# Optimization experiments

Measured on AMD Instinct MI355X. Metric: run time of the kernel, lower is better.

The kernel has to match this reference:

```python
import jax, jax.numpy as jnp
import numpy as np

TOKENS = 8192
IN_F = 4096
OUT_F = 4096
ZERO_POINT = 0  # int8 activation zero point (module default)


def setup_inputs() -> dict:
    key = jax.random.key(0)
    k1, k2, k3, k4 = jax.random.split(key, 4)
    # int8-valued activations/weights stored as int32 (same math as torch upcast path)
    x = jax.random.randint(k1, (TOKENS, IN_F), 0, 127, dtype=jnp.int32)
    weight = jax.random.randint(k2, (IN_F, OUT_F), -127, 127, dtype=jnp.int32)
    bias = jax.random.randint(k3, (1, OUT_F), -64, 64, dtype=jnp.int32)
    gemm_scales = jax.random.uniform(k4, (1, OUT_F), dtype=jnp.float32) * 1e-3
    return {"x": x, "weight": weight, "bias": bias, "gemm_scales": gemm_scales}


def reference(x, weight, bias, gemm_scales):
    # adjust_a = (x - zero_point), upcast to float32 like the torch module
    adjust_a = (x - ZERO_POINT).astype(jnp.float32)          # [T, in]
    w = weight.astype(jnp.float32)                           # [in, out]
    gemm_o = (adjust_a @ w + bias.astype(jnp.float32)) * gemm_scales  # [T, out]
    return gemm_o
```

## Files before the change

kernel.cpp:

```cpp
#include <hip/hip_runtime.h>

using i32x4 = __attribute__((ext_vector_type(4))) int;

#define AS3(p) ((__attribute__((address_space(3))) void*)(p))
#define AS1(p) ((const __attribute__((address_space(1))) void*)(p))

constexpr int M = 8192;
constexpr int N = 4096;
constexpr int K = 4096;
constexpr int BK = 64;
constexpr int NT = K / BK;
constexpr int NBUF = 4;

__global__ void pack_a_kernel(const int4* __restrict__ x, unsigned* __restrict__ a8, int nUnits) {
    int stride = gridDim.x * blockDim.x;
    for (int u = blockIdx.x * blockDim.x + threadIdx.x; u < nUnits; u += stride) {
        int4 v = x[u];
        a8[u] = (v.x & 255) | ((v.y & 255) << 8) | ((v.z & 255) << 16) | (v.w << 24);
    }
}

__global__ void pack_wT_kernel(const int* __restrict__ w, char* __restrict__ b8t) {
    __shared__ __align__(16) char T[64][80];
    const int n0 = blockIdx.x * 64;
    const int k0 = blockIdx.y * 64;
    const int tid = threadIdx.x;

    #pragma unroll
    for (int i = 0; i < 4; i++) {
        int u = tid + i * 256;
        int r = u >> 4;
        int c = u & 15;
        int4 v = *(const int4*)&w[(size_t)(k0 + r) * N + n0 + 4 * c];
        T[4 * c + 0][r] = (char)v.x;
        T[4 * c + 1][r] = (char)v.y;
        T[4 * c + 2][r] = (char)v.z;
        T[4 * c + 3][r] = (char)v.w;
    }
    __syncthreads();

    const int n = tid >> 2;
    const int q = tid & 3;
    int4 val = *(const int4*)&T[n][16 * q];
    *(int4*)&b8t[(size_t)(n0 + n) * K + k0 + 16 * q] = val;
}

__global__ __launch_bounds__(512, 1) void gemm_i8_kernel(
    const char* __restrict__ a8, const char* __restrict__ b8t,
    const int* __restrict__ bias, const float* __restrict__ scales,
    float* __restrict__ out)
{
    __shared__ __align__(16) char As[NBUF][256 * BK];
    __shared__ __align__(16) char Bs[NBUF][256 * BK];

    const int tid  = threadIdx.x;
    const int lane = tid & 63;
    const int wid  = tid >> 6;
    const int wr   = wid >> 2;
    const int wc   = wid & 3;

    const int bid = blockIdx.x;
    const int xcd = bid & 7;
    const int l   = bid >> 3;
    const int tm  = (xcd >> 1) * 8 + (l >> 3);
    const int tn  = (xcd & 1) * 8 + (l & 7);
    const size_t brow = (size_t)tm * 256;
    const size_t bcol = (size_t)tn * 256;

    const int srow = tid >> 2;
    const int schS = ((tid & 3) ^ ((tid >> 3) & 3)) << 4;
    const char* aG = a8  + (brow + srow) * (size_t)K + schS;
    const char* bG = b8t + (bcol + srow) * (size_t)K + schS;
    const int ldsW = wid * 1024;

    i32x4 acc[8][4];
    #pragma unroll
    for (int m = 0; m < 8; m++)
        #pragma unroll
        for (int n = 0; n < 4; n++)
            #pragma unroll
            for (int r = 0; r < 4; r++)
                acc[m][n][r] = 0;

    auto stage = [&](int slot, int kt) {
        const char* a = aG + (size_t)kt * BK;
        const char* b = bG + (size_t)kt * BK;
        char* Ad = &As[slot][0] + ldsW;
        char* Bd = &Bs[slot][0] + ldsW;
        __builtin_amdgcn_global_load_lds(AS1(a),                  AS3(Ad),        16, 0, 0);
        __builtin_amdgcn_global_load_lds(AS1(a + (size_t)128*K),  AS3(Ad + 8192), 16, 0, 0);
        __builtin_amdgcn_global_load_lds(AS1(b),                  AS3(Bd),        16, 0, 0);
        __builtin_amdgcn_global_load_lds(AS1(b + (size_t)128*K),  AS3(Bd + 8192), 16, 0, 0);
    };

    const int frow  = lane & 15;
    const int c0sw  = ((lane >> 4) ^ ((frow >> 1) & 3)) << 4;
    const int raOff = wr * 8192 + frow * 64 + c0sw;
    const int rbOff = wc * 4096 + frow * 64 + c0sw;

    stage(0, 0);
    stage(1, 1);
    stage(2, 2);
    asm volatile("s_waitcnt vmcnt(8)" ::: "memory");
    __builtin_amdgcn_s_barrier();

    #pragma unroll 4
    for (int t = 0; t < NT; ++t) {
        const int slot = t & 3;
        if (t + 3 < NT) stage((t + 3) & 3, t + 3);

        const char* Ab = &As[slot][0] + raOff;
        const char* Bb = &Bs[slot][0] + rbOff;

        i32x4 bfr[4], afr[8];
        #pragma unroll
        for (int n = 0; n < 4; ++n)
            bfr[n] = *(const i32x4*)(Bb + n * 1024);
        #pragma unroll
        for (int m = 0; m < 8; ++m)
            afr[m] = *(const i32x4*)(Ab + m * 1024);

        __builtin_amdgcn_s_barrier();

        asm volatile("s_waitcnt lgkmcnt(4)" ::: "memory");
        __builtin_amdgcn_sched_barrier(0);
        __builtin_amdgcn_s_setprio(1);
        #pragma unroll
        for (int m = 0; m < 4; ++m)
            #pragma unroll
            for (int n = 0; n < 4; ++n)
                acc[m][n] = __builtin_amdgcn_mfma_i32_16x16x64_i8(afr[m], bfr[n], acc[m][n], 0, 0, 0);
        __builtin_amdgcn_s_setprio(0);
        __builtin_amdgcn_sched_barrier(0);

        asm volatile("s_waitcnt lgkmcnt(0)" ::: "memory");
        __builtin_amdgcn_sched_barrier(0);
        __builtin_amdgcn_s_setprio(1);
        #pragma unroll
        for (int m = 4; m < 8; ++m)
            #pragma unroll
            for (int n = 0; n < 4; ++n)
                acc[m][n] = __builtin_amdgcn_mfma_i32_16x16x64_i8(afr[m], bfr[n], acc[m][n], 0, 0, 0);
        __builtin_amdgcn_s_setprio(0);
        __builtin_amdgcn_sched_barrier(0);

        if (t <= NT - 4) asm volatile("s_waitcnt vmcnt(8)" ::: "memory");
        else             asm volatile("s_waitcnt vmcnt(0)" ::: "memory");
        __builtin_amdgcn_s_barrier();
    }

    #pragma unroll
    for (int n = 0; n < 4; ++n) {
        const int col = (int)bcol + wc * 64 + n * 16 + (lane & 15);
        const int bv  = bias[col];
        const float sv = scales[col];
        #pragma unroll
        for (int m = 0; m < 8; ++m) {
            const size_t row0 = brow + wr * 128 + m * 16 + ((lane >> 4) << 2);
            float* o = out + row0 * (size_t)N + col;
            #pragma unroll
            for (int r = 0; r < 4; ++r)
                o[(size_t)r * N] = (float)(acc[m][n][r] + bv) * sv;
        }
    }
}

extern "C" void kernel_launch(void* const* d_in, const int* in_sizes, int n_in,
                              void* d_out, int out_size, void* d_ws, size_t ws_size,
                              hipStream_t stream) {
    const int*   x      = (const int*)d_in[0];
    const int*   w      = (const int*)d_in[1];
    const int*   bias   = (const int*)d_in[2];
    const float* scales = (const float*)d_in[3];
    float* out = (float*)d_out;

    char* a8  = (char*)d_ws;
    char* b8t = a8 + (size_t)M * K;

    pack_a_kernel<<<2048, 256, 0, stream>>>((const int4*)x, (unsigned*)a8, M * K / 4);

    dim3 gt(N / 64, K / 64);
    pack_wT_kernel<<<gt, 256, 0, stream>>>(w, b8t);

    gemm_i8_kernel<<<(M / 256) * (N / 256), 512, 0, stream>>>(a8, b8t, bias, scales, out);
}
```

Before: 206.4 us.

## Restructure int8 GEMM mainloop to BK=128 double buffer with interleaved quadrant MFMA phases

Doubles the K tile to 128 and replaces the 4-deep LDS ring with a double buffer. Each iteration is split into four MFMA quadrant phases, with barriers between them and fragment loads interleaved so that A/B reads reuse registers. The next tile's global-to-LDS loads are issued in two halves between phases. The aim is fewer loop iterations, a smaller fragment register footprint, and higher occupancy (launch bounds now allow 2 waves per SIMD). The cost is many more barriers per iteration, a full vmcnt(0) drain at the end of each iteration, and a shallower prefetch distance.

```diff
diff --git a/kernel.cpp b/kernel.cpp
--- a/kernel.cpp
+++ b/kernel.cpp
@@ -8,9 +8,8 @@
 constexpr int M = 8192;
 constexpr int N = 4096;
 constexpr int K = 4096;
-constexpr int BK = 64;
+constexpr int BK = 128;
 constexpr int NT = K / BK;
-constexpr int NBUF = 4;
 
 __global__ void pack_a_kernel(const int4* __restrict__ x, unsigned* __restrict__ a8, int nUnits) {
     int stride = gridDim.x * blockDim.x;
@@ -45,13 +44,13 @@
     *(int4*)&b8t[(size_t)(n0 + n) * K + k0 + 16 * q] = val;
 }
 
-__global__ __launch_bounds__(512, 1) void gemm_i8_kernel(
+__global__ __launch_bounds__(512, 2) void gemm_i8_kernel(
     const char* __restrict__ a8, const char* __restrict__ b8t,
     const int* __restrict__ bias, const float* __restrict__ scales,
     float* __restrict__ out)
 {
-    __shared__ __align__(16) char As[NBUF][256 * BK];
-    __shared__ __align__(16) char Bs[NBUF][256 * BK];
+    __shared__ __align__(16) char As[2][256 * BK];
+    __shared__ __align__(16) char Bs[2][256 * BK];
 
     const int tid  = threadIdx.x;
     const int lane = tid & 63;
@@ -67,11 +66,11 @@
     const size_t brow = (size_t)tm * 256;
     const size_t bcol = (size_t)tn * 256;
 
-    const int srow = tid >> 2;
-    const int schS = ((tid & 3) ^ ((tid >> 3) & 3)) << 4;
-    const char* aG = a8  + (brow + srow) * (size_t)K + schS;
-    const char* bG = b8t + (bcol + srow) * (size_t)K + schS;
-    const int ldsW = wid * 1024;
+    const int srowS = (wid << 3) + (lane >> 3);
+    const int schS  = ((lane & 7) ^ (lane >> 3)) << 4;
+    const char* aGs = a8  + (brow + srowS) * (size_t)K + schS;
+    const char* bGs = b8t + (bcol + srowS) * (size_t)K + schS;
+    const int ldsU = wid * 1024;
 
     i32x4 acc[8][4];
     #pragma unroll
@@ -82,70 +81,108 @@
             for (int r = 0; r < 4; r++)
                 acc[m][n][r] = 0;
 
-    auto stage = [&](int slot, int kt) {
-        const char* a = aG + (size_t)kt * BK;
-        const char* b = bG + (size_t)kt * BK;
-        char* Ad = &As[slot][0] + ldsW;
-        char* Bd = &Bs[slot][0] + ldsW;
-        __builtin_amdgcn_global_load_lds(AS1(a),                  AS3(Ad),        16, 0, 0);
-        __builtin_amdgcn_global_load_lds(AS1(a + (size_t)128*K),  AS3(Ad + 8192), 16, 0, 0);
-        __builtin_amdgcn_global_load_lds(AS1(b),                  AS3(Bd),        16, 0, 0);
-        __builtin_amdgcn_global_load_lds(AS1(b + (size_t)128*K),  AS3(Bd + 8192), 16, 0, 0);
+    auto stageA = [&](int b, int u, int kt) {
+        __builtin_amdgcn_global_load_lds(AS1(aGs + (size_t)(u * 64) * K + (size_t)kt * BK),
+                                         AS3(&As[b][u * 8192 + ldsU]), 16, 0, 0);
     };
+    auto stageB = [&](int b, int u, int kt) {
+        __builtin_amdgcn_global_load_lds(AS1(bGs + (size_t)(u * 64) * K + (size_t)kt * BK),
+                                         AS3(&Bs[b][u * 8192 + ldsU]), 16, 0, 0);
+    };
 
     const int frow  = lane & 15;
-    const int c0sw  = ((lane >> 4) ^ ((frow >> 1) & 3)) << 4;
-    const int raOff = wr * 8192 + frow * 64 + c0sw;
-    const int rbOff = wc * 4096 + frow * 64 + c0sw;
-
-    stage(0, 0);
-    stage(1, 1);
-    stage(2, 2);
-    asm volatile("s_waitcnt vmcnt(8)" ::: "memory");
+    const int c0sw  = ((lane >> 4) ^ (lane & 7)) << 4;
+    const int c1sw  = c0sw ^ 64;
+    const int raBase = wr * 16384 + frow * BK;
+    const int rbBase = wc * 8192  + frow * BK;
+
+    #pragma unroll
+    for (int u = 0; u < 4; ++u) { stageA(0, u, 0); stageB(0, u, 0); }
+    asm volatile("s_waitcnt vmcnt(0)" ::: "memory");
     __builtin_amdgcn_s_barrier();
 
-    #pragma unroll 4
+    i32x4 aq[4][2], b0[2][2], b1[2][2];
+
     for (int t = 0; t < NT; ++t) {
-        const int slot = t & 3;
-        if (t + 3 < NT) stage((t + 3) & 3, t + 3);
-
-        const char* Ab = &As[slot][0] + raOff;
-        const char* Bb = &Bs[slot][0] + rbOff;
-
-        i32x4 bfr[4], afr[8];
-        #pragma unroll
-        for (int n = 0; n < 4; ++n)
-            bfr[n] = *(const i32x4*)(Bb + n * 1024);
-        #pragma unroll
-        for (int m = 0; m < 8; ++m)
-            afr[m] = *(const i32x4*)(Ab + m * 1024);
-
-        __builtin_amdgcn_s_barrier();
-
-        asm volatile("s_waitcnt lgkmcnt(4)" ::: "memory");
-        __builtin_amdgcn_sched_barrier(0);
-        __builtin_amdgcn_s_setprio(1);
-        #pragma unroll
-        for (int m = 0; m < 4; ++m)
-            #pragma unroll
-            for (int n = 0; n < 4; ++n)
-                acc[m][n] = __builtin_amdgcn_mfma_i32_16x16x64_i8(afr[m], bfr[n], acc[m][n], 0, 0, 0);
-        __builtin_amdgcn_s_setprio(0);
-        __builtin_amdgcn_sched_barrier(0);
-
+        const int s = t & 1;
+        const int o = s ^ 1;
+        const char* Ab = &As[s][0] + raBase;
+        const char* Bb = &Bs[s][0] + rbBase;
+
+        if (t + 1 < NT) { stageA(o, 0, t + 1); stageA(o, 1, t + 1); stageB(o, 0, t + 1); stageB(o, 1, t + 1); }
+        #pragma unroll
+        for (int n = 0; n < 2; ++n) {
+            b0[n][0] = *(const i32x4*)(Bb + n * 2048 + c0sw);
+            b0[n][1] = *(const i32x4*)(Bb + n * 2048 + c1sw);
+        }
+        #pragma unroll
+        for (int m = 0; m < 4; ++m) {
+            aq[m][0] = *(const i32x4*)(Ab + m * 2048 + c0sw);
+            aq[m][1] = *(const i32x4*)(Ab + m * 2048 + c1sw);
+        }
+        __builtin_amdgcn_s_barrier();
         asm volatile("s_waitcnt lgkmcnt(0)" ::: "memory");
         __builtin_amdgcn_sched_barrier(0);
         __builtin_amdgcn_s_setprio(1);
         #pragma unroll
-        for (int m = 4; m < 8; ++m)
-            #pragma unroll
-            for (int n = 0; n < 4; ++n)
-                acc[m][n] = __builtin_amdgcn_mfma_i32_16x16x64_i8(afr[m], bfr[n], acc[m][n], 0, 0, 0);
-        __builtin_amdgcn_s_setprio(0);
+        for (int m = 0; m < 4; ++m)
+            #pragma unroll
+            for (int n = 0; n < 2; ++n) {
+                acc[m][n] = __builtin_amdgcn_mfma_i32_16x16x64_i8(aq[m][0], b0[n][0], acc[m][n], 0, 0, 0);
+                acc[m][n] = __builtin_amdgcn_mfma_i32_16x16x64_i8(aq[m][1], b0[n][1], acc[m][n], 0, 0, 0);
+            }
+        __builtin_amdgcn_s_setprio(0);
+        __builtin_amdgcn_s_barrier();
+
+        if (t + 1 < NT) { stageA(o, 2, t + 1); stageA(o, 3, t + 1); stageB(o, 2, t + 1); stageB(o, 3, t + 1); }
+        #pragma unroll
+        for (int n = 0; n < 2; ++n) {
+            b1[n][0] = *(const i32x4*)(Bb + (2 + n) * 2048 + c0sw);
+            b1[n][1] = *(const i32x4*)(Bb + (2 + n) * 2048 + c1sw);
+        }
+        __builtin_amdgcn_s_barrier();
+        asm volatile("s_waitcnt lgkmcnt(0)" ::: "memory");
         __builtin_amdgcn_sched_barrier(0);
-
-        if (t <= NT - 4) asm volatile("s_waitcnt vmcnt(8)" ::: "memory");
-        else             asm volatile("s_waitcnt vmcnt(0)" ::: "memory");
+        __builtin_amdgcn_s_setprio(1);
+        #pragma unroll
+        for (int m = 0; m < 4; ++m)
+            #pragma unroll
+            for (int n = 0; n < 2; ++n) {
+                acc[m][2 + n] = __builtin_amdgcn_mfma_i32_16x16x64_i8(aq[m][0], b1[n][0], acc[m][2 + n], 0, 0, 0);
+                acc[m][2 + n] = __builtin_amdgcn_mfma_i32_16x16x64_i8(aq[m][1], b1[n][1], acc[m][2 + n], 0, 0, 0);
+            }
+        __builtin_amdgcn_s_setprio(0);
+        __builtin_amdgcn_s_barrier();
+
+        #pragma unroll
+        for (int m = 0; m < 4; ++m) {
+            aq[m][0] = *(const i32x4*)(Ab + 8192 + m * 2048 + c0sw);
+            aq[m][1] = *(const i32x4*)(Ab + 8192 + m * 2048 + c1sw);
+        }
+        __builtin_amdgcn_s_barrier();
+        asm volatile("s_waitcnt lgkmcnt(0)" ::: "memory");
+        __builtin_amdgcn_sched_barrier(0);
+        __builtin_amdgcn_s_setprio(1);
+        #pragma unroll
+        for (int m = 0; m < 4; ++m)
+            #pragma unroll
+            for (int n = 0; n < 2; ++n) {
+                acc[4 + m][2 + n] = __builtin_amdgcn_mfma_i32_16x16x64_i8(aq[m][0], b1[n][0], acc[4 + m][2 + n], 0, 0, 0);
+                acc[4 + m][2 + n] = __builtin_amdgcn_mfma_i32_16x16x64_i8(aq[m][1], b1[n][1], acc[4 + m][2 + n], 0, 0, 0);
+            }
+        __builtin_amdgcn_s_setprio(0);
+        __builtin_amdgcn_s_barrier();
+
+        __builtin_amdgcn_s_setprio(1);
+        #pragma unroll
+        for (int m = 0; m < 4; ++m)
+            #pragma unroll
+            for (int n = 0; n < 2; ++n) {
+                acc[4 + m][n] = __builtin_amdgcn_mfma_i32_16x16x64_i8(aq[m][0], b0[n][0], acc[4 + m][n], 0, 0, 0);
+                acc[4 + m][n] = __builtin_amdgcn_mfma_i32_16x16x64_i8(aq[m][1], b0[n][1], acc[4 + m][n], 0, 0, 0);
+            }
+        __builtin_amdgcn_s_setprio(0);
+        asm volatile("s_waitcnt vmcnt(0)" ::: "memory");
         __builtin_amdgcn_s_barrier();
     }
 
```

New measurement: 238.3 us. +15.4%, slower.
